# Performance work log

Measured on AMD Instinct MI355X. Metric: run time of the kernel, lower is better.

Reference implementation:

```python
import jax, jax.numpy as jnp
import numpy as np
import math
from jax import lax

B, L = 64, 8192
S = L // 8          # width after 3 stride-(1,2) SAME convs
D = 4 * 5           # height(4) * channels(5) -> per-token feature dim
D_FLAT = S * D


def setup_inputs():
    key = jax.random.key(0)
    ks = jax.random.split(key, 32)
    sc = 0.1
    inp = {
        "inputs": jax.random.randint(ks[0], (B, L), 0, 4, dtype=jnp.int32),
        # conv stack: HWIO kernels, Conv2D(5,(4,4),(1,2),'SAME')
        "conv_w1": sc * jax.random.normal(ks[1], (4, 4, 1, 5), jnp.float32),
        "conv_b1": jnp.zeros((5,), jnp.float32),
        "conv_w2": sc * jax.random.normal(ks[2], (4, 4, 5, 5), jnp.float32),
        "conv_b2": jnp.zeros((5,), jnp.float32),
        "conv_w3": sc * jax.random.normal(ks[3], (4, 4, 5, 5), jnp.float32),
        "conv_b3": jnp.zeros((5,), jnp.float32),
        # 3 SelfAttn blocks, each with K/Q/V projections [D, D]
        "attn1_K": sc * jax.random.normal(ks[4], (D, D), jnp.float32),
        "attn1_Q": sc * jax.random.normal(ks[5], (D, D), jnp.float32),
        "attn1_V": sc * jax.random.normal(ks[6], (D, D), jnp.float32),
        "attn2_K": sc * jax.random.normal(ks[7], (D, D), jnp.float32),
        "attn2_Q": sc * jax.random.normal(ks[8], (D, D), jnp.float32),
        "attn2_V": sc * jax.random.normal(ks[9], (D, D), jnp.float32),
        "attn3_K": sc * jax.random.normal(ks[10], (D, D), jnp.float32),
        "attn3_Q": sc * jax.random.normal(ks[11], (D, D), jnp.float32),
        "attn3_V": sc * jax.random.normal(ks[12], (D, D), jnp.float32),
        # 3 Dense(10) layers (no activation, as in Keras defaults)
        "dense_w1": 0.01 * jax.random.normal(ks[13], (D_FLAT, 10), jnp.float32),
        "dense_b1": jnp.zeros((10,), jnp.float32),
        "dense_w2": sc * jax.random.normal(ks[14], (10, 10), jnp.float32),
        "dense_b2": jnp.zeros((10,), jnp.float32),
        "dense_w3": sc * jax.random.normal(ks[15], (10, 10), jnp.float32),
        "dense_b3": jnp.zeros((10,), jnp.float32),
    }
    return inp


def _conv(x, w, b):
    # NHWC, HWIO, strides (1,2), SAME
    y = lax.conv_general_dilated(x, w, window_strides=(1, 2), padding="SAME",
                                 dimension_numbers=("NHWC", "HWIO", "NHWC"))
    return y + b


def _self_attn(x, Kw, Qw, Vw):
    # x: [B, S, D]; manual causal scaled dot-product attention
    K = x @ Kw
    Q = x @ Qw
    V = x @ Vw
    s = Q.shape[1]
    mask = jnp.triu(jnp.full((s, s), -jnp.inf, dtype=x.dtype), k=1)
    scores = jnp.einsum("bsd,btd->bst", Q, K) / math.sqrt(K.shape[-1]) + mask
    return jax.nn.softmax(scores, axis=-1) @ V


def reference(inputs, conv_w1, conv_b1, conv_w2, conv_b2, conv_w3, conv_b3,
              attn1_K, attn1_Q, attn1_V, attn2_K, attn2_Q, attn2_V,
              attn3_K, attn3_Q, attn3_V,
              dense_w1, dense_b1, dense_w2, dense_b2, dense_w3, dense_b3):
    # one_hot over axis=1 -> [B, 4, L], then channel dim -> [B, 4, L, 1]
    x = jax.nn.one_hot(inputs, 4, axis=1, dtype=jnp.float32)[..., None]
    x = _conv(x, conv_w1, conv_b1)
    x = _conv(x, conv_w2, conv_b2)
    x = _conv(x, conv_w3, conv_b3)            # [B, 4, S, 5]
    # tokens along width, features = height(4) x channels(5)
    x = jnp.transpose(x, (0, 2, 1, 3)).reshape(x.shape[0], S, D)
    x = _self_attn(x, attn1_K, attn1_Q, attn1_V)
    x = _self_attn(x, attn2_K, attn2_Q, attn2_V)
    x = _self_attn(x, attn3_K, attn3_Q, attn3_V)
    x = x.reshape(x.shape[0], -1)             # flatten [B, S*D]
    x = x @ dense_w1 + dense_b1
    x = x @ dense_w2 + dense_b2
    x = x @ dense_w3 + dense_b3               # [B, 10]
    return x
```

## Files before the change

### kernel.cpp

```cpp
#include <hip/hip_runtime.h>
#include <hip/hip_bf16.h>


#define B_ 64
#define L_ 8192
#define S_ 1024
#define D_ 20

typedef unsigned short ushort_t;
typedef __attribute__((ext_vector_type(8))) short short8_t;
typedef __attribute__((ext_vector_type(4))) float f32x4_t;

__device__ __forceinline__ ushort_t f2bf(float f) {
  unsigned u = __float_as_uint(f);
  return (ushort_t)((u + 0x7fffu + ((u >> 16) & 1u)) >> 16);
}
__device__ __forceinline__ float bf2f(ushort_t h) {
  return __uint_as_float(((unsigned)h) << 16);
}

__global__ __launch_bounds__(256) void conv12_kernel(
    const int* __restrict__ inp,
    const float* __restrict__ W1c, const float* __restrict__ B1c,
    const float* __restrict__ W2c, const float* __restrict__ B2c,
    float* __restrict__ out,
    const float* __restrict__ W1d,
    float* __restrict__ W1T) {
  __shared__ float w1s[80], b1s[5], w2s[400], b2s[5];
  for (int j = threadIdx.x; j < 400; j += 256) w2s[j] = W2c[j];
  if (threadIdx.x < 80)      w1s[threadIdx.x]      = W1c[threadIdx.x];
  else if (threadIdx.x < 85) b1s[threadIdx.x - 80] = B1c[threadIdx.x - 80];
  else if (threadIdx.x < 90) b2s[threadIdx.x - 85] = B2c[threadIdx.x - 85];
  __syncthreads();
  const int idx = blockIdx.x * 256 + threadIdx.x;
  const int b  = idx >> 11;
  const int wo = idx & 2047;
  const int* ib = inp + (size_t)b * L_;
  int iv[10];
#pragma unroll
  for (int t = 0; t < 10; ++t) {
    int g = 4 * wo - 3 + t;
    iv[t] = (g >= 0 && g < L_) ? ib[g] : -100;
  }
  float val[4][4][5];
#pragma unroll
  for (int pos = 0; pos < 4; ++pos) {
    const int w1 = 2 * wo - 1 + pos;
    const bool okp = (w1 >= 0 && w1 < 4096);
#pragma unroll
    for (int hi = 0; hi < 4; ++hi)
#pragma unroll
      for (int ci = 0; ci < 5; ++ci) val[hi][pos][ci] = okp ? b1s[ci] : 0.f;
    if (okp) {
#pragma unroll
      for (int kw = 0; kw < 4; ++kw) {
        const int gw = 2 * w1 - 1 + kw;
        if (gw >= 0 && gw < L_) {
          const int v = iv[2 * pos + kw];
#pragma unroll
          for (int hi = 0; hi < 4; ++hi) {
            const int kh = v - hi + 1;
            if (kh >= 0 && kh < 4) {
#pragma unroll
              for (int ci = 0; ci < 5; ++ci)
                val[hi][pos][ci] += w1s[(kh * 4 + kw) * 5 + ci];
            }
          }
        }
      }
    }
  }
  float acc[4][5];
#pragma unroll
  for (int h = 0; h < 4; ++h)
#pragma unroll
    for (int c = 0; c < 5; ++c) acc[h][c] = b2s[c];
#pragma unroll
  for (int kh = 0; kh < 4; ++kh)
#pragma unroll
    for (int kw = 0; kw < 4; ++kw)
#pragma unroll
      for (int ci = 0; ci < 5; ++ci) {
        const float* wp = w2s + ((kh * 4 + kw) * 5 + ci) * 5;
        float w0 = wp[0], w1v = wp[1], w2v = wp[2], w3 = wp[3], w4 = wp[4];
#pragma unroll
        for (int h = 0; h < 4; ++h) {
          int hi = h - 1 + kh;
          if (hi >= 0 && hi < 4) {
            float x = val[hi][kw][ci];
            acc[h][0] += w0 * x;  acc[h][1] += w1v * x; acc[h][2] += w2v * x;
            acc[h][3] += w3 * x;  acc[h][4] += w4 * x;
          }
        }
      }
  float* ob = out + (size_t)b * 4 * 2048 * 5;
#pragma unroll
  for (int h = 0; h < 4; ++h)
#pragma unroll
    for (int c = 0; c < 5; ++c) ob[(h * 2048 + wo) * 5 + c] = acc[h][c];
  for (int j = idx; j < 204800; j += 131072) {
    int col = j / 20480, i2 = j - col * 20480;
    W1T[j] = W1d[i2 * 10 + col];
  }
}

__global__ __launch_bounds__(256) void conv3_proj_kernel(
    const float* __restrict__ in,
    const float* __restrict__ W,  const float* __restrict__ Bi,
    const float* __restrict__ Kw, const float* __restrict__ Qw,
    const float* __restrict__ Vw,
    ushort_t* __restrict__ Qb, ushort_t* __restrict__ Kb,
    ushort_t* __restrict__ Vt) {
  constexpr int WIN = 2048;
  __shared__ float ws[400], bs[5];
  __shared__ float kw[400], qw[400], vw[400];
  for (int j = threadIdx.x; j < 400; j += 256) {
    ws[j] = W[j]; kw[j] = Kw[j]; qw[j] = Qw[j]; vw[j] = Vw[j];
  }
  if (threadIdx.x < 5) bs[threadIdx.x] = Bi[threadIdx.x];
  __syncthreads();
  const int r  = blockIdx.x * 256 + threadIdx.x;
  const int b  = r >> 10;
  const int wo = r & 1023;
  float val[4][4][5];
#pragma unroll
  for (int hi = 0; hi < 4; ++hi) {
    const float* ir = in + ((size_t)b * 4 + hi) * WIN * 5;
#pragma unroll
    for (int kwp = 0; kwp < 4; ++kwp) {
      int wi = 2 * wo - 1 + kwp;
      bool ok = (wi >= 0 && wi < WIN);
#pragma unroll
      for (int ci = 0; ci < 5; ++ci) val[hi][kwp][ci] = ok ? ir[wi * 5 + ci] : 0.f;
    }
  }
  float acc[4][5];
#pragma unroll
  for (int h = 0; h < 4; ++h)
#pragma unroll
    for (int c = 0; c < 5; ++c) acc[h][c] = bs[c];
#pragma unroll
  for (int kh = 0; kh < 4; ++kh)
#pragma unroll
    for (int kwp = 0; kwp < 4; ++kwp)
#pragma unroll
      for (int ci = 0; ci < 5; ++ci) {
        const float* wp = ws + ((kh * 4 + kwp) * 5 + ci) * 5;
        float w0 = wp[0], w1 = wp[1], w2 = wp[2], w3 = wp[3], w4 = wp[4];
#pragma unroll
        for (int h = 0; h < 4; ++h) {
          int hi = h - 1 + kh;
          if (hi >= 0 && hi < 4) {
            float x = val[hi][kwp][ci];
            acc[h][0] += w0 * x; acc[h][1] += w1 * x; acc[h][2] += w2 * x;
            acc[h][3] += w3 * x; acc[h][4] += w4 * x;
          }
        }
      }
  float x[D_];
#pragma unroll
  for (int h = 0; h < 4; ++h)
#pragma unroll
    for (int c = 0; c < 5; ++c) x[h * 5 + c] = acc[h][c];
  float q[D_], k[D_], v[D_];
#pragma unroll
  for (int j = 0; j < D_; ++j) { q[j] = 0.f; k[j] = 0.f; v[j] = 0.f; }
#pragma unroll
  for (int i = 0; i < D_; ++i) {
#pragma unroll
    for (int j = 0; j < D_; ++j) {
      q[j] += x[i] * qw[i * D_ + j];
      k[j] += x[i] * kw[i * D_ + j];
      v[j] += x[i] * vw[i * D_ + j];
    }
  }
  const float sc = 0.22360679774997896f;
  ushort_t qt[32], kt[32];
#pragma unroll
  for (int j = 0; j < D_; ++j) { qt[j] = f2bf(q[j] * sc); kt[j] = f2bf(k[j]); }
#pragma unroll
  for (int j = D_; j < 32; ++j) { qt[j] = 0; kt[j] = 0; }
  int4* qd = (int4*)(Qb + (size_t)r * 32);
  int4* kd = (int4*)(Kb + (size_t)r * 32);
#pragma unroll
  for (int j = 0; j < 4; ++j) {
    qd[j] = *(const int4*)(qt + 8 * j);
    kd[j] = *(const int4*)(kt + 8 * j);
  }
  ushort_t* vbase = Vt + ((size_t)b * 32) * 1024 + wo;
#pragma unroll
  for (int d = 0; d < D_; ++d) vbase[d * 1024] = f2bf(v[d]);
}

#define TT_ 128
template <bool FUSE>
__global__ __launch_bounds__(256) void attn_kernel(
    const ushort_t* __restrict__ Qb, const ushort_t* __restrict__ Kb,
    const ushort_t* __restrict__ Vt,
    const float* __restrict__ Kw2, const float* __restrict__ Qw2,
    const float* __restrict__ Vw2,
    ushort_t* __restrict__ Qb2, ushort_t* __restrict__ Kb2,
    ushort_t* __restrict__ Vt2,
    const float* __restrict__ W1T,
    float* __restrict__ part2) {
  const int b     = blockIdx.y;
  const int strip = (blockIdx.x + 4 * (blockIdx.y >> 4)) & 15;
  const int q0    = strip * 64;
  const int tid   = threadIdx.x;
  const int w     = tid >> 6;
  const int lane  = tid & 63;
  const int n     = lane & 15;
  const int quad  = lane >> 4;
  const int qbase = q0 + 16 * w;
  __shared__ ushort_t kts[128 * 40];
  __shared__ ushort_t vts[32 * 136];
  __shared__ ushort_t pts[4][16 * 40];
  __shared__ float extraf[FUSE ? 2480 : 3840];
  if (FUSE) {
    float tmp[5];
#pragma unroll
    for (int u = 0; u < 5; ++u) {
      int j = tid + u * 256;
      if (j < 1200) {
        int m = j / 400, oo = j - m * 400;
        tmp[u] = (m == 0) ? Kw2[oo] : (m == 1) ? Qw2[oo] : Vw2[oo];
      }
    }
#pragma unroll
    for (int u = 0; u < 5; ++u) {
      int j = tid + u * 256;
      if (j < 1200) extraf[j] = tmp[u];
    }
  }
  const ushort_t* KbB = Kb + (size_t)b * 1024 * 32;
  const ushort_t* VtB = Vt + (size_t)b * 32 * 1024;
  short8_t qfrag = *(const short8_t*)(Qb + ((size_t)(b * 1024 + qbase + n)) * 32 + quad * 8);
  f32x4_t oA = {0.f, 0.f, 0.f, 0.f};
  f32x4_t oB = {0.f, 0.f, 0.f, 0.f};
  f32x4_t lac = {0.f, 0.f, 0.f, 0.f};
  const f32x4_t zero = {0.f, 0.f, 0.f, 0.f};
  const int nt = q0 + 64;
  ushort_t* prow = pts[w];
  for (int t0 = 0; t0 < nt; t0 += TT_) {
    __syncthreads();
    for (int i = tid; i < 512; i += 256) {
      int row = i >> 2, qc = i & 3;
      *(int4*)(kts + row * 40 + qc * 8) =
          *(const int4*)(KbB + (size_t)(t0 + row) * 32 + qc * 8);
    }
    for (int i = tid; i < 320; i += 256) {
      int row = i >> 4, cc = i & 15;
      *(int4*)(vts + row * 136 + cc * 8) =
          *(const int4*)(VtB + (size_t)row * 1024 + t0 + cc * 8);
    }
    __syncthreads();
    short8_t kf[4][2];
#pragma unroll
    for (int cc = 0; cc < 4; ++cc) {
      kf[cc][0] = *(const short8_t*)(kts + (cc * 32 + n) * 40 + quad * 8);
      kf[cc][1] = *(const short8_t*)(kts + (cc * 32 + 16 + n) * 40 + quad * 8);
    }
#pragma unroll
    for (int cc = 0; cc < 4; ++cc) {
      const int tc = t0 + cc * 32;
      f32x4_t sA = __builtin_amdgcn_mfma_f32_16x16x32_bf16(qfrag, kf[cc][0], zero, 0, 0, 0);
      f32x4_t sB = __builtin_amdgcn_mfma_f32_16x16x32_bf16(qfrag, kf[cc][1], zero, 0, 0, 0);
#pragma unroll
      for (int r = 0; r < 4; ++r) {
        const int qg = qbase + quad * 4 + r;
        float pA = (tc + n      <= qg) ? __expf(sA[r]) : 0.f;
        float pB = (tc + 16 + n <= qg) ? __expf(sB[r]) : 0.f;
        ushort_t hA = f2bf(pA), hB = f2bf(pB);
        lac[r] += bf2f(hA) + bf2f(hB);
        prow[(quad * 4 + r) * 40 + n]      = hA;
        prow[(quad * 4 + r) * 40 + 16 + n] = hB;
      }
      __asm__ volatile("s_waitcnt lgkmcnt(0)" ::: "memory");
      short8_t pfrag = *(const short8_t*)(prow + n * 40 + quad * 8);
      const short8_t vfA = *(const short8_t*)(vts + n * 136 + cc * 32 + quad * 8);
      const short8_t vfB = *(const short8_t*)(vts + (16 + n) * 136 + cc * 32 + quad * 8);
      oA = __builtin_amdgcn_mfma_f32_16x16x32_bf16(pfrag, vfA, oA, 0, 0, 0);
      oB = __builtin_amdgcn_mfma_f32_16x16x32_bf16(pfrag, vfB, oB, 0, 0, 0);
    }
  }
#pragma unroll
  for (int m = 1; m <= 8; m <<= 1) {
#pragma unroll
    for (int r = 0; r < 4; ++r) lac[r] += __shfl_xor(lac[r], m, 64);
  }
  if (FUSE) {
    float* pw  = extraf;
    float* oxw = extraf + 1200 + w * 320;
#pragma unroll
    for (int r = 0; r < 4; ++r) {
      const float inv = 1.f / lac[r];
      const int qq = quad * 4 + r;
      oxw[qq * 20 + n] = oA[r] * inv;
      if (n < 4) oxw[qq * 20 + 16 + n] = oB[r] * inv;
    }
    __asm__ volatile("s_waitcnt lgkmcnt(0)" ::: "memory");
    const int row  = lane >> 2;
    const int part = lane & 3;
    float x[D_];
#pragma unroll
    for (int i = 0; i < D_; ++i) x[i] = oxw[row * 20 + i];
    float qv[5], kv[5], vv[5];
#pragma unroll
    for (int jj = 0; jj < 5; ++jj) { qv[jj] = 0.f; kv[jj] = 0.f; vv[jj] = 0.f; }
#pragma unroll
    for (int i = 0; i < D_; ++i) {
      const float xi = x[i];
#pragma unroll
      for (int jj = 0; jj < 5; ++jj) {
        const int j = 5 * part + jj;
        kv[jj] += xi * pw[i * 20 + j];
        qv[jj] += xi * pw[400 + i * 20 + j];
        vv[jj] += xi * pw[800 + i * 20 + j];
      }
    }
    const float sc = 0.22360679774997896f;
    const int rg = b * 1024 + qbase + row;
    const int s  = rg & 1023;
#pragma unroll
    for (int jj = 0; jj < 5; ++jj) {
      const int j = 5 * part + jj;
      Kb2[(size_t)rg * 32 + j] = f2bf(kv[jj]);
      Qb2[(size_t)rg * 32 + j] = f2bf(qv[jj] * sc);
      Vt2[(size_t)b * 32768 + (size_t)j * 1024 + s] = f2bf(vv[jj]);
    }
    if (part == 0) {
#pragma unroll
      for (int u = 0; u < 6; ++u)
        *(unsigned*)(Kb2 + (size_t)rg * 32 + 20 + 2 * u) = 0u;
    } else if (part == 1) {
#pragma unroll
      for (int u = 0; u < 6; ++u)
        *(unsigned*)(Qb2 + (size_t)rg * 32 + 20 + 2 * u) = 0u;
    }
  } else {
    float* oxflat = extraf;
    float* oxw    = oxflat + w * 320;
    float* red    = extraf + 1280;
#pragma unroll
    for (int r = 0; r < 4; ++r) {
      const float inv = 1.f / lac[r];
      const int qq = quad * 4 + r;
      oxw[qq * 20 + n] = oA[r] * inv;
      if (n < 4) oxw[qq * 20 + 16 + n] = oB[r] * inv;
    }
    __syncthreads();
    float acc[10];
#pragma unroll
    for (int j = 0; j < 10; ++j) acc[j] = 0.f;
    const float* wb = W1T;
    const int base = q0 * 20;
#pragma unroll
    for (int k = 0; k < 5; ++k) {
      const int il = tid + 256 * k;
      const float xv = oxflat[il];
#pragma unroll
      for (int j = 0; j < 10; ++j)
        acc[j] += xv * wb[(size_t)j * 20480 + base + il];
    }
#pragma unroll
    for (int j = 0; j < 10; ++j) red[tid * 10 + j] = acc[j];
    __syncthreads();
    for (int off = 128; off > 0; off >>= 1) {
      if (tid < off) {
#pragma unroll
        for (int j = 0; j < 10; ++j) red[tid * 10 + j] += red[(tid + off) * 10 + j];
      }
      __syncthreads();
    }
    if (tid < 10) part2[((b << 4) + strip) * 10 + tid] = red[tid];
  }
}

__global__ __launch_bounds__(64) void dense_final(
    const float* __restrict__ part2,
    const float* __restrict__ B1,
    const float* __restrict__ W2, const float* __restrict__ B2,
    const float* __restrict__ W3, const float* __restrict__ B3,
    float* __restrict__ out) {
  const int b = blockIdx.x;
  __shared__ float y1[10], y2[10];
  if (threadIdx.x < 10) {
    int j = threadIdx.x;
    float s = 0.f;
#pragma unroll
    for (int st = 0; st < 16; ++st) s += part2[((b << 4) + st) * 10 + j];
    y1[j] = s + B1[j];
  }
  __syncthreads();
  if (threadIdx.x < 10) {
    int j = threadIdx.x;
    float s = B2[j];
#pragma unroll
    for (int i = 0; i < 10; ++i) s += y1[i] * W2[i * 10 + j];
    y2[j] = s;
  }
  __syncthreads();
  if (threadIdx.x < 10) {
    int j = threadIdx.x;
    float s = B3[j];
#pragma unroll
    for (int i = 0; i < 10; ++i) s += y2[i] * W3[i * 10 + j];
    out[b * 10 + j] = s;
  }
}

extern "C" void kernel_launch(void* const* d_in, const int* in_sizes, int n_in,
                              void* d_out, int out_size, void* d_ws, size_t ws_size,
                              hipStream_t stream) {
  const int*   inp = (const int*)d_in[0];
  const float* cw1 = (const float*)d_in[1];
  const float* cb1 = (const float*)d_in[2];
  const float* cw2 = (const float*)d_in[3];
  const float* cb2 = (const float*)d_in[4];
  const float* cw3 = (const float*)d_in[5];
  const float* cb3 = (const float*)d_in[6];
  const float* a1K = (const float*)d_in[7];
  const float* a1Q = (const float*)d_in[8];
  const float* a1V = (const float*)d_in[9];
  const float* a2K = (const float*)d_in[10];
  const float* a2Q = (const float*)d_in[11];
  const float* a2V = (const float*)d_in[12];
  const float* a3K = (const float*)d_in[13];
  const float* a3Q = (const float*)d_in[14];
  const float* a3V = (const float*)d_in[15];
  const float* dw1 = (const float*)d_in[16];
  const float* db1 = (const float*)d_in[17];
  const float* dw2 = (const float*)d_in[18];
  const float* db2 = (const float*)d_in[19];
  const float* dw3 = (const float*)d_in[20];
  const float* db3 = (const float*)d_in[21];
  float* outp = (float*)d_out;

  float* wsf = (float*)d_ws;
  ushort_t* qbA  = (ushort_t*)(wsf);
  ushort_t* kbA  = (ushort_t*)(wsf + 1048576);
  ushort_t* vtA  = (ushort_t*)(wsf + 2097152);
  float*    part2= wsf + 4456448;
  float*    w1t  = wsf + 4466688;
  ushort_t* qbB  = (ushort_t*)(wsf + 4671488);
  ushort_t* kbB  = (ushort_t*)(wsf + 5712384);
  ushort_t* vtB  = (ushort_t*)(wsf + 6760960);
  float*    c2   = wsf + 5242880;

  conv12_kernel<<<512, 256, 0, stream>>>(inp, cw1, cb1, cw2, cb2, c2, dw1, w1t);

  conv3_proj_kernel<<<256, 256, 0, stream>>>(c2, cw3, cb3, a1K, a1Q, a1V, qbA, kbA, vtA);
  attn_kernel<true><<<dim3(16, 64), 256, 0, stream>>>(
      qbA, kbA, vtA, a2K, a2Q, a2V, qbB, kbB, vtB, nullptr, nullptr);
  attn_kernel<true><<<dim3(16, 64), 256, 0, stream>>>(
      qbB, kbB, vtB, a3K, a3Q, a3V, qbA, kbA, vtA, nullptr, nullptr);
  attn_kernel<false><<<dim3(16, 64), 256, 0, stream>>>(
      qbA, kbA, vtA, nullptr, nullptr, nullptr, nullptr, nullptr, nullptr,
      w1t, part2);

  dense_final<<<64, 64, 0, stream>>>(part2, db1, dw2, db2, dw3, db3, outp);
}
```

Before: 238.7 us.

## Compute transposed scores so P feeds PV MFMA directly from registers

Swaps operand order in the QK^T MFMA so each lane holds a column of scores (keys × queries), letting the bf16 probabilities be packed in registers and fed straight into 16x16x16 MFMAs for the PV product. This removes the per-wave LDS staging buffer for P, its store/waitcnt/reload round trip, and simplifies the row-sum reduction to two shuffles. In exchange it issues twice as many smaller MFMAs (16x16x16 instead of 16x16x32) and changes the output register layout for the epilogue writes.

Measured after the change: 217.7 us. 8.8% less time.

```diff
diff --git a/kernel.cpp b/kernel.cpp
--- a/kernel.cpp
+++ b/kernel.cpp
@@ -9,6 +9,7 @@
 
 typedef unsigned short ushort_t;
 typedef __attribute__((ext_vector_type(8))) short short8_t;
+typedef __attribute__((ext_vector_type(4))) short short4_t;
 typedef __attribute__((ext_vector_type(4))) float f32x4_t;
 
 __device__ __forceinline__ ushort_t f2bf(float f) {
@@ -212,9 +213,9 @@
   const int n     = lane & 15;
   const int quad  = lane >> 4;
   const int qbase = q0 + 16 * w;
+  const int qg    = qbase + n;
   __shared__ ushort_t kts[128 * 40];
   __shared__ ushort_t vts[32 * 136];
-  __shared__ ushort_t pts[4][16 * 40];
   __shared__ float extraf[FUSE ? 2480 : 3840];
   if (FUSE) {
     float tmp[5];
@@ -237,10 +238,9 @@
   short8_t qfrag = *(const short8_t*)(Qb + ((size_t)(b * 1024 + qbase + n)) * 32 + quad * 8);
   f32x4_t oA = {0.f, 0.f, 0.f, 0.f};
   f32x4_t oB = {0.f, 0.f, 0.f, 0.f};
-  f32x4_t lac = {0.f, 0.f, 0.f, 0.f};
+  float lsum = 0.f;
   const f32x4_t zero = {0.f, 0.f, 0.f, 0.f};
   const int nt = q0 + 64;
-  ushort_t* prow = pts[w];
   for (int t0 = 0; t0 < nt; t0 += TT_) {
     __syncthreads();
     for (int i = tid; i < 512; i += 256) {
@@ -254,49 +254,41 @@
           *(const int4*)(VtB + (size_t)row * 1024 + t0 + cc * 8);
     }
     __syncthreads();
-    short8_t kf[4][2];
-#pragma unroll
-    for (int cc = 0; cc < 4; ++cc) {
-      kf[cc][0] = *(const short8_t*)(kts + (cc * 32 + n) * 40 + quad * 8);
-      kf[cc][1] = *(const short8_t*)(kts + (cc * 32 + 16 + n) * 40 + quad * 8);
-    }
-#pragma unroll
-    for (int cc = 0; cc < 4; ++cc) {
-      const int tc = t0 + cc * 32;
-      f32x4_t sA = __builtin_amdgcn_mfma_f32_16x16x32_bf16(qfrag, kf[cc][0], zero, 0, 0, 0);
-      f32x4_t sB = __builtin_amdgcn_mfma_f32_16x16x32_bf16(qfrag, kf[cc][1], zero, 0, 0, 0);
+    short8_t kf[8];
+#pragma unroll
+    for (int hc = 0; hc < 8; ++hc)
+      kf[hc] = *(const short8_t*)(kts + (hc * 16 + n) * 40 + quad * 8);
+#pragma unroll
+    for (int hc = 0; hc < 8; ++hc) {
+      const int tg = t0 + hc * 16 + quad * 4;
+      f32x4_t s = __builtin_amdgcn_mfma_f32_16x16x32_bf16(kf[hc], qfrag, zero, 0, 0, 0);
+      ushort_t pk4[4];
 #pragma unroll
       for (int r = 0; r < 4; ++r) {
-        const int qg = qbase + quad * 4 + r;
-        float pA = (tc + n      <= qg) ? __expf(sA[r]) : 0.f;
-        float pB = (tc + 16 + n <= qg) ? __expf(sB[r]) : 0.f;
-        ushort_t hA = f2bf(pA), hB = f2bf(pB);
-        lac[r] += bf2f(hA) + bf2f(hB);
-        prow[(quad * 4 + r) * 40 + n]      = hA;
-        prow[(quad * 4 + r) * 40 + 16 + n] = hB;
-      }
-      __asm__ volatile("s_waitcnt lgkmcnt(0)" ::: "memory");
-      short8_t pfrag = *(const short8_t*)(prow + n * 40 + quad * 8);
-      const short8_t vfA = *(const short8_t*)(vts + n * 136 + cc * 32 + quad * 8);
-      const short8_t vfB = *(const short8_t*)(vts + (16 + n) * 136 + cc * 32 + quad * 8);
-      oA = __builtin_amdgcn_mfma_f32_16x16x32_bf16(pfrag, vfA, oA, 0, 0, 0);
-      oB = __builtin_amdgcn_mfma_f32_16x16x32_bf16(pfrag, vfB, oB, 0, 0, 0);
-    }
-  }
-#pragma unroll
-  for (int m = 1; m <= 8; m <<= 1) {
-#pragma unroll
-    for (int r = 0; r < 4; ++r) lac[r] += __shfl_xor(lac[r], m, 64);
-  }
+        float p = (tg + r <= qg) ? __expf(s[r]) : 0.f;
+        ushort_t h = f2bf(p);
+        lsum += bf2f(h);
+        pk4[r] = h;
+      }
+      short4_t pfrag = *(const short4_t*)pk4;
+      short4_t vlo = *(const short4_t*)(vts + n * 136 + hc * 16 + quad * 4);
+      short4_t vhi = *(const short4_t*)(vts + (16 + n) * 136 + hc * 16 + quad * 4);
+      oA = __builtin_amdgcn_mfma_f32_16x16x16bf16_1k(vlo, pfrag, oA, 0, 0, 0);
+      oB = __builtin_amdgcn_mfma_f32_16x16x16bf16_1k(vhi, pfrag, oB, 0, 0, 0);
+    }
+  }
+  float l = lsum;
+  l += __shfl_xor(l, 16, 64);
+  l += __shfl_xor(l, 32, 64);
+  const float inv = 1.f / l;
   if (FUSE) {
     float* pw  = extraf;
     float* oxw = extraf + 1200 + w * 320;
 #pragma unroll
-    for (int r = 0; r < 4; ++r) {
-      const float inv = 1.f / lac[r];
-      const int qq = quad * 4 + r;
-      oxw[qq * 20 + n] = oA[r] * inv;
-      if (n < 4) oxw[qq * 20 + 16 + n] = oB[r] * inv;
+    for (int r = 0; r < 4; ++r) oxw[n * 20 + quad * 4 + r] = oA[r] * inv;
+    if (quad == 0) {
+#pragma unroll
+      for (int r = 0; r < 4; ++r) oxw[n * 20 + 16 + r] = oB[r] * inv;
     }
     __asm__ volatile("s_waitcnt lgkmcnt(0)" ::: "memory");
     const int row  = lane >> 2;
@@ -342,11 +334,10 @@
     float* oxw    = oxflat + w * 320;
     float* red    = extraf + 1280;
 #pragma unroll
-    for (int r = 0; r < 4; ++r) {
-      const float inv = 1.f / lac[r];
-      const int qq = quad * 4 + r;
-      oxw[qq * 20 + n] = oA[r] * inv;
-      if (n < 4) oxw[qq * 20 + 16 + n] = oB[r] * inv;
+    for (int r = 0; r < 4; ++r) oxw[n * 20 + quad * 4 + r] = oA[r] * inv;
+    if (quad == 0) {
+#pragma unroll
+      for (int r = 0; r < 4; ++r) oxw[n * 20 + 16 + r] = oB[r] * inv;
     }
     __syncthreads();
     float acc[10];
```
